# Kernel optimization log

Measured on AMD Instinct MI355X. Metric: run time of the kernel, lower is better.

The kernel has to match this reference:

```python
import jax, jax.numpy as jnp
import numpy as np
from jax import lax

T = 6  # max_message_length


def setup_inputs() -> dict:
    key = jax.random.key(0)
    ks = jax.random.split(key, 10)
    B, VIS, H, E, V = 8192, 512, 256, 64, 4096
    s = lambda k, shp, fan: jax.random.normal(k, shp, jnp.float32) * (1.0 / np.sqrt(fan))
    return {
        "vision_feat": jax.random.normal(ks[0], (B, VIS), jnp.float32),
        "Wv": s(ks[1], (VIS, H), VIS),
        "bv": jnp.zeros((H,), jnp.float32),
        "gru_kernel": s(ks[2], (E, 3 * H), E),          # input kernel [z|r|h]
        "gru_rec_kernel": s(ks[3], (H, 3 * H), H),      # recurrent kernel [z|r|h]
        "gru_bias_in": jnp.zeros((3 * H,), jnp.float32),
        "gru_bias_rec": jnp.zeros((3 * H,), jnp.float32),
        "Wo": s(ks[4], (H, V), H),
        "bo": jnp.zeros((V,), jnp.float32),
        "emb": s(ks[5], (V, E), E),
    }


def _gru_cell(x, h, k, rk, b_in, b_rec):
    # Keras GRUCell, reset_after=True
    H = h.shape[1]
    xm = x @ k + b_in          # [B, 3H]
    hm = h @ rk + b_rec        # [B, 3H]
    xz, xr, xh = xm[:, :H], xm[:, H:2 * H], xm[:, 2 * H:]
    hz, hr, hh = hm[:, :H], hm[:, H:2 * H], hm[:, 2 * H:]
    z = jax.nn.sigmoid(xz + hz)
    r = jax.nn.sigmoid(xr + hr)
    hh_t = jnp.tanh(xh + r * hh)
    return z * h + (1.0 - z) * hh_t


def reference(vision_feat, Wv, bv, gru_kernel, gru_rec_kernel, gru_bias_in,
              gru_bias_rec, Wo, bo, emb):
    B = vision_feat.shape[0]
    # NOTE: original code never feeds h_t back as GRU state; state is fixed.
    prev_hidden = vision_feat @ Wv + bv            # [B, H]
    cell0 = jnp.zeros((B, emb.shape[1]), vision_feat.dtype)

    def step(cell_input, _):
        h = _gru_cell(cell_input, prev_hidden, gru_kernel, gru_rec_kernel,
                      gru_bias_in, gru_bias_rec)
        lp = jax.nn.log_softmax(h @ Wo + bo, axis=1)      # [B, V]
        ent = -jnp.sum(lp * jnp.exp(lp), axis=1)          # [B]
        sym = jnp.argmax(lp, axis=1)                      # greedy (training=False)
        sel = jnp.take_along_axis(lp, sym[:, None], axis=1)[:, 0]
        return emb[sym], (sym, sel, ent, h)

    _, (syms, sels, ents, hs) = lax.scan(step, cell0, None, length=T)
    sequence = syms.T.astype(jnp.float32)                 # [B, T]
    logits = sels.T                                       # [B, T]
    entropy = jnp.mean(ents, axis=0)                      # [B]
    message_length = jnp.full((B,), float(T), jnp.float32)
    h_t = hs[-1]                                          # [B, H]
    return sequence, logits, entropy, message_length, h_t
```

## Files before the change

kernel.cpp:

```cpp
#include <hip/hip_runtime.h>
#include <hip/hip_fp16.h>
#include <math.h>


typedef __attribute__((ext_vector_type(8))) _Float16 half8v;
typedef __attribute__((ext_vector_type(4))) float f32x4;

__device__ __forceinline__ int lds_off(int row, int slot) {
    return (row << 6) + ((slot ^ (row & 3) ^ ((row >> 2) & 3)) << 4);
}

__device__ __forceinline__ void gld_lds16(const void* src, void* dst) {
    __builtin_amdgcn_global_load_lds(
        (const __attribute__((address_space(1))) void*)src,
        (__attribute__((address_space(3))) void*)dst, 16, 0, 0);
}

template<int C>
__device__ __forceinline__ float dppf(float x) {
    return __builtin_bit_cast(float, __builtin_amdgcn_update_dpp(
        __builtin_bit_cast(int, x), __builtin_bit_cast(int, x), C, 0xF, 0xF, false));
}
template<int C>
__device__ __forceinline__ int dppi(int x) {
    return __builtin_amdgcn_update_dpp(x, x, C, 0xF, 0xF, false);
}

__device__ __forceinline__ void f16split(float v, unsigned short& u0,
                                         unsigned short& u1) {
    __half a = __float2half(v);
    float f = __half2float(a);
    __half b = __float2half(v - f);
    u0 = __half_as_ushort(a);
    u1 = __half_as_ushort(b);
}

__device__ __forceinline__ float fast_tanh(float x) {
    float t = __expf(-2.0f * fabsf(x));
    float th = (1.0f - t) / (1.0f + t);
    return copysignf(th, x);
}

__global__ __launch_bounds__(256) void split_ew(
    const float* __restrict__ in, unsigned short* __restrict__ o0,
    unsigned short* __restrict__ o1, int n4)
{
    int i = blockIdx.x * 256 + threadIdx.x;
    if (i >= n4) return;
    float4 v = *(const float4*)&in[(size_t)i * 4];
    unsigned short a[4], b[4];
    f16split(v.x, a[0], b[0]); f16split(v.y, a[1], b[1]);
    f16split(v.z, a[2], b[2]); f16split(v.w, a[3], b[3]);
    *(uint2*)&o0[(size_t)i * 4] = *(uint2*)a;
    *(uint2*)&o1[(size_t)i * 4] = *(uint2*)b;
}

__global__ __launch_bounds__(256) void trans_split(
    const float* __restrict__ W, unsigned short* __restrict__ o0,
    unsigned short* __restrict__ o1, int N, int K)
{
    __shared__ float Ts[64][65];
    const int tid = threadIdx.x;
    const int n0 = blockIdx.x * 64, k0 = blockIdx.y * 64;
    const int ty = tid >> 2, tx = tid & 3;
    #pragma unroll
    for (int q = 0; q < 4; ++q) {
        float4 v = *(const float4*)&W[(size_t)(k0 + ty) * N + n0 + tx * 16 + q * 4];
        Ts[ty][tx * 16 + q * 4 + 0] = v.x; Ts[ty][tx * 16 + q * 4 + 1] = v.y;
        Ts[ty][tx * 16 + q * 4 + 2] = v.z; Ts[ty][tx * 16 + q * 4 + 3] = v.w;
    }
    __syncthreads();
    #pragma unroll
    for (int ii = 0; ii < 2; ++ii) {
        int item = tid + (ii << 8);
        int n = item >> 3, g = item & 7;
        unsigned short u0[8], u1[8];
        #pragma unroll
        for (int e = 0; e < 8; ++e)
            f16split(Ts[g * 8 + e][n], u0[e], u1[e]);
        size_t base = (size_t)(n0 + n) * K + k0 + g * 8;
        *(uint4*)&o0[base] = *(uint4*)u0;
        *(uint4*)&o1[base] = *(uint4*)u1;
    }
}

template<int KTOT, bool SPLIT>
__global__ __launch_bounds__(256) void mfma_gemm(
    const unsigned short* __restrict__ a0s, const unsigned short* __restrict__ a1s,
    const unsigned short* __restrict__ b0s, const unsigned short* __restrict__ b1s,
    const float* __restrict__ bias, float* __restrict__ C, int ldc,
    unsigned short* __restrict__ s0, unsigned short* __restrict__ s1)
{
    __shared__ char lds[16384];
    const int tid = threadIdx.x;
    const int w = tid >> 6, lane = tid & 63;
    const int c16 = lane & 15, rg = lane >> 4;
    const int m0 = blockIdx.y << 6, n0 = blockIdx.x << 6;
    const int arow0 = (w >> 1) << 5, brow0 = (w & 1) << 5;

    const unsigned short* segsrc = (w == 0) ? a0s : (w == 1) ? a1s
                                 : (w == 2) ? b0s : b1s;
    const int segrow0 = (w < 2) ? m0 : n0;

    f32x4 acc[2][2] = {};

    for (int t = 0; t < KTOT / 32; ++t) {
        const int k0 = t << 5;
        #pragma unroll
        for (int q = 0; q < 4; ++q) {
            int row = (q << 4) + (lane >> 2);
            int slot = (lane & 3) ^ (row & 3) ^ ((row >> 2) & 3);
            gld_lds16(segsrc + (size_t)(segrow0 + row) * KTOT + k0 + (slot << 3),
                      &lds[(w << 12) + (q << 10)]);
        }
        asm volatile("s_waitcnt vmcnt(0)" ::: "memory");
        __syncthreads();
        half8v afr[2][2], bfr[2][2];
        #pragma unroll
        for (int i = 0; i < 2; ++i) {
            int oa = lds_off(arow0 + (i << 4) + c16, rg);
            afr[i][0] = *(half8v*)&lds[oa];
            afr[i][1] = *(half8v*)&lds[4096 + oa];
            int ob = lds_off(brow0 + (i << 4) + c16, rg);
            bfr[i][0] = *(half8v*)&lds[8192 + ob];
            bfr[i][1] = *(half8v*)&lds[12288 + ob];
        }
        #pragma unroll
        for (int i = 0; i < 2; ++i)
            #pragma unroll
            for (int j = 0; j < 2; ++j) {
                f32x4 c = acc[i][j];
                c = __builtin_amdgcn_mfma_f32_16x16x32_f16(afr[i][0], bfr[j][0], c, 0, 0, 0);
                c = __builtin_amdgcn_mfma_f32_16x16x32_f16(afr[i][1], bfr[j][0], c, 0, 0, 0);
                c = __builtin_amdgcn_mfma_f32_16x16x32_f16(afr[i][0], bfr[j][1], c, 0, 0, 0);
                acc[i][j] = c;
            }
        __syncthreads();
    }

    #pragma unroll
    for (int j = 0; j < 2; ++j) {
        int col = n0 + brow0 + (j << 4) + c16;
        float bb = bias[col];
        #pragma unroll
        for (int i = 0; i < 2; ++i)
            #pragma unroll
            for (int reg = 0; reg < 4; ++reg) {
                int row = m0 + arow0 + (i << 4) + (rg << 2) + reg;
                float v = acc[i][j][reg] + bb;
                C[(size_t)row * ldc + col] = v;
                if (SPLIT) {
                    unsigned short u0, u1;
                    f16split(v, u0, u1);
                    s0[(size_t)row * ldc + col] = u0;
                    s1[(size_t)row * ldc + col] = u1;
                }
            }
    }
}

__global__ __launch_bounds__(256) void gru_fused(
    const float4* __restrict__ pstats, const float* __restrict__ emb,
    const float* __restrict__ gk, const float* __restrict__ b_in,
    const float* __restrict__ hm, const float* __restrict__ ph,
    unsigned short* __restrict__ h0, unsigned short* __restrict__ h1,
    float* __restrict__ ht_out, float* __restrict__ out_seq,
    float* __restrict__ out_sel, float* __restrict__ out_ent, int t)
{
    __shared__ float xsT[64][8];
    __shared__ int syms_lds[8];
    const int tid = threadIdx.x;
    const int row0 = blockIdx.x * 8;
    float az[8], ar[8], ah[8];
    const float bz = b_in[tid], br = b_in[256 + tid], bh = b_in[512 + tid];
    #pragma unroll
    for (int r = 0; r < 8; ++r) { az[r] = bz; ar[r] = br; ah[r] = bh; }

    if (t > 0) {
        const int r = tid >> 5, p = tid & 31;
        const int row = row0 + r;
        float4 pa = pstats[(size_t)p * 8192 + row];
        float4 pb = pstats[(size_t)(p + 32) * 8192 + row];
        float M = pa.x, S = pa.y + pb.y, Q = pa.z + pb.z;
        int A = __float_as_int(pa.w);
        { int a2 = __float_as_int(pb.w);
          if (pb.x > M || (pb.x == M && a2 < A)) { M = pb.x; A = a2; } }
        #pragma unroll
        for (int off = 1; off < 32; off <<= 1) {
            float m2 = __shfl_xor(M, off);
            float s2 = __shfl_xor(S, off);
            float q2 = __shfl_xor(Q, off);
            int   a2 = __shfl_xor(A, off);
            S += s2; Q += q2;
            if (m2 > M || (m2 == M && a2 < A)) { M = m2; A = a2; }
        }
        if (p == 0) {
            float lse = __logf(S);
            float sel = M - lse;
            float ent = lse - Q / S;
            out_seq[(size_t)row * 6 + (t - 1)] = (float)A;
            out_sel[(size_t)row * 6 + (t - 1)] = sel;
            float ea = (t == 1) ? ent : (out_ent[row] + ent);
            out_ent[row] = ea;
            syms_lds[r] = A;
        }
        __syncthreads();
        for (int l = tid; l < 512; l += 256) {
            int r2 = l >> 6, e = l & 63;
            xsT[e][r2] = emb[(size_t)syms_lds[r2] * 64 + e];
        }
        __syncthreads();
        #pragma unroll 4
        for (int e = 0; e < 64; ++e) {
            float kz  = gk[e * 768 + tid];
            float kr_ = gk[e * 768 + 256 + tid];
            float kh  = gk[e * 768 + 512 + tid];
            float4 x0 = *(float4*)&xsT[e][0];
            float4 x1 = *(float4*)&xsT[e][4];
            float xv[8] = {x0.x, x0.y, x0.z, x0.w, x1.x, x1.y, x1.z, x1.w};
            #pragma unroll
            for (int r2 = 0; r2 < 8; ++r2) {
                az[r2] = fmaf(xv[r2], kz, az[r2]);
                ar[r2] = fmaf(xv[r2], kr_, ar[r2]);
                ah[r2] = fmaf(xv[r2], kh, ah[r2]);
            }
        }
    }
    #pragma unroll
    for (int r = 0; r < 8; ++r) {
        const int row = row0 + r;
        float hz  = hm[(size_t)row * 768 + tid];
        float hr  = hm[(size_t)row * 768 + 256 + tid];
        float hh  = hm[(size_t)row * 768 + 512 + tid];
        float phv = ph[(size_t)row * 256 + tid];
        float z  = 1.0f / (1.0f + __expf(-(az[r] + hz)));
        float rr = 1.0f / (1.0f + __expf(-(ar[r] + hr)));
        float ht = fast_tanh(ah[r] + rr * hh);
        float hv = z * phv + (1.0f - z) * ht;
        size_t idx = (size_t)row * 256 + tid;
        unsigned short u0, u1;
        f16split(hv, u0, u1);
        h0[idx] = u0; h1[idx] = u1;
        if (ht_out) ht_out[idx] = hv;
    }
}

__global__ __launch_bounds__(256, 3) void logits_mfma(
    const unsigned short* __restrict__ h0, const unsigned short* __restrict__ h1,
    const unsigned short* __restrict__ w0, const unsigned short* __restrict__ w1,
    const float* __restrict__ bo, float4* __restrict__ pstats)
{
    __shared__ char lds[32768];
    const int tid = threadIdx.x;
    const int w = tid >> 6, lane = tid & 63;
    const int c16 = lane & 15, rg = lane >> 4;
    const int m0 = blockIdx.y << 7, n0 = blockIdx.x << 7;
    const int arow0 = (w >> 1) << 6, brow0 = (w & 1) << 6;

    const unsigned short* segsrc = (w == 0) ? h0 : (w == 1) ? h1
                                 : (w == 2) ? w0 : w1;
    const int segrow0 = (w < 2) ? m0 : n0;

    f32x4 acc[4][4] = {};

    for (int t = 0; t < 8; ++t) {
        const int k0 = t << 5;
        #pragma unroll
        for (int q = 0; q < 8; ++q) {
            int row = (q << 4) + (lane >> 2);
            int slot = (lane & 3) ^ (row & 3) ^ ((row >> 2) & 3);
            gld_lds16(segsrc + (size_t)(segrow0 + row) * 256 + k0 + (slot << 3),
                      &lds[(w << 13) + (q << 10)]);
        }
        asm volatile("s_waitcnt vmcnt(0)" ::: "memory");
        __syncthreads();
        half8v afr[4][2];
        #pragma unroll
        for (int i = 0; i < 4; ++i) {
            int o = lds_off(arow0 + (i << 4) + c16, rg);
            afr[i][0] = *(half8v*)&lds[o];
            afr[i][1] = *(half8v*)&lds[8192 + o];
        }
        #pragma unroll
        for (int j = 0; j < 4; ++j) {
            int o = lds_off(brow0 + (j << 4) + c16, rg);
            half8v b0 = *(half8v*)&lds[16384 + o];
            half8v b1 = *(half8v*)&lds[24576 + o];
            #pragma unroll
            for (int i = 0; i < 4; ++i) {
                f32x4 c = acc[i][j];
                c = __builtin_amdgcn_mfma_f32_16x16x32_f16(afr[i][0], b0, c, 0, 0, 0);
                c = __builtin_amdgcn_mfma_f32_16x16x32_f16(afr[i][1], b0, c, 0, 0, 0);
                c = __builtin_amdgcn_mfma_f32_16x16x32_f16(afr[i][0], b1, c, 0, 0, 0);
                acc[i][j] = c;
            }
        }
        __syncthreads();
    }

    const int wn0 = n0 + brow0;
    float bov[4];
    #pragma unroll
    for (int j = 0; j < 4; ++j) bov[j] = bo[wn0 + j * 16 + c16];
    #pragma unroll
    for (int i = 0; i < 4; ++i) {
        #pragma unroll
        for (int reg = 0; reg < 4; ++reg) {
            float l0 = acc[i][0][reg] + bov[0];
            float l1 = acc[i][1][reg] + bov[1];
            float l2 = acc[i][2][reg] + bov[2];
            float l3 = acc[i][3][reg] + bov[3];
            float m = l0; int a = wn0 + c16;
            if (l1 > m) { m = l1; a = wn0 + 16 + c16; }
            if (l2 > m) { m = l2; a = wn0 + 32 + c16; }
            if (l3 > m) { m = l3; a = wn0 + 48 + c16; }
            float e0 = __expf(l0), e1 = __expf(l1), e2 = __expf(l2), e3 = __expf(l3);
            float s = (e0 + e1) + (e2 + e3);
            float q = fmaf(l0, e0, fmaf(l1, e1, fmaf(l2, e2, l3 * e3)));
            s += dppf<0x108>(s); s += dppf<0x104>(s);
            s += dppf<0x102>(s); s += dppf<0x101>(s);
            q += dppf<0x108>(q); q += dppf<0x104>(q);
            q += dppf<0x102>(q); q += dppf<0x101>(q);
            #define MMERGE(C) { float m2 = dppf<C>(m); int a2 = dppi<C>(a); \
                bool bt = (m2 > m) || (m2 == m && a2 < a); \
                m = bt ? m2 : m; a = bt ? a2 : a; }
            MMERGE(0x108) MMERGE(0x104) MMERGE(0x102) MMERGE(0x101)
            #undef MMERGE
            if (c16 == 0) {
                int grow = m0 + arow0 + (i << 4) + (rg << 2) + reg;
                pstats[(size_t)((blockIdx.x << 1) + (w & 1)) * 8192 + grow] =
                    make_float4(m, s, q, __int_as_float(a));
            }
        }
    }
}

__global__ __launch_bounds__(64) void finalize_kernel(
    const float4* __restrict__ pstats, float* __restrict__ out_seq,
    float* __restrict__ out_sel, float* __restrict__ out_ent,
    float* __restrict__ out_ml)
{
    const int row = blockIdx.x * 64 + threadIdx.x;
    float M = -INFINITY, S = 0.f, Q = 0.f; int A = 0;
    #pragma unroll 8
    for (int p = 0; p < 64; ++p) {
        float4 pp = pstats[(size_t)p * 8192 + row];
        S += pp.y; Q += pp.z;
        int a2 = __float_as_int(pp.w);
        if (pp.x > M || (pp.x == M && a2 < A)) { M = pp.x; A = a2; }
    }
    float lse = __logf(S);
    float sel = M - lse;
    float ent = lse - Q / S;
    out_seq[(size_t)row * 6 + 5] = (float)A;
    out_sel[(size_t)row * 6 + 5] = sel;
    out_ent[row] = (out_ent[row] + ent) * (1.0f / 6.0f);
    out_ml[row] = 6.0f;
}

extern "C" void kernel_launch(void* const* d_in, const int* in_sizes, int n_in,
                              void* d_out, int out_size, void* d_ws, size_t ws_size,
                              hipStream_t stream) {
    const float* vis  = (const float*)d_in[0];
    const float* Wv   = (const float*)d_in[1];
    const float* bv   = (const float*)d_in[2];
    const float* gk   = (const float*)d_in[3];
    const float* grk  = (const float*)d_in[4];
    const float* bin  = (const float*)d_in[5];
    const float* brec = (const float*)d_in[6];
    const float* Wo   = (const float*)d_in[7];
    const float* bo   = (const float*)d_in[8];
    const float* emb  = (const float*)d_in[9];

    float* out = (float*)d_out;
    float* out_seq = out;
    float* out_sel = out + 49152;
    float* out_ent = out + 98304;
    float* out_ml  = out + 106496;
    float* out_ht  = out + 114688;

    char* ws = (char*)d_ws;
    float*          ph     = (float*)(ws);
    float*          hm     = (float*)(ws + 8388608);
    unsigned short* vis0   = (unsigned short*)(ws + 8388608);
    unsigned short* vis1   = (unsigned short*)(ws + 16777216);
    unsigned short* h0     = (unsigned short*)(ws + 33554432);
    unsigned short* h1     = (unsigned short*)(ws + 37748736);
    unsigned short* w0     = (unsigned short*)(ws + 41943040);
    unsigned short* w1     = (unsigned short*)(ws + 44040192);
    float4*         pstats = (float4*)(ws + 46137344);
    unsigned short* ph0    = (unsigned short*)(ws + 46137344);
    unsigned short* ph1    = (unsigned short*)(ws + 50331648);
    unsigned short* wv0    = (unsigned short*)(ws + 54558720);
    unsigned short* wv1    = (unsigned short*)(ws + 54820864);
    unsigned short* g0     = (unsigned short*)(ws + 55083008);
    unsigned short* g1     = (unsigned short*)(ws + 55476224);

    trans_split<<<dim3(64, 4), 256, 0, stream>>>(Wo, w0, w1, 4096, 256);
    trans_split<<<dim3(4, 8), 256, 0, stream>>>(Wv, wv0, wv1, 256, 512);
    trans_split<<<dim3(12, 4), 256, 0, stream>>>(grk, g0, g1, 768, 256);
    split_ew<<<4096, 256, 0, stream>>>(vis, vis0, vis1, 1048576);

    mfma_gemm<512, true><<<dim3(4, 128), 256, 0, stream>>>(
        vis0, vis1, wv0, wv1, bv, ph, 256, ph0, ph1);
    mfma_gemm<256, false><<<dim3(12, 128), 256, 0, stream>>>(
        ph0, ph1, g0, g1, brec, hm, 768, nullptr, nullptr);

    for (int t = 0; t < 6; ++t) {
        gru_fused<<<1024, 256, 0, stream>>>(pstats, emb, gk, bin, hm, ph,
                                            h0, h1,
                                            (t == 5) ? out_ht : nullptr,
                                            out_seq, out_sel, out_ent, t);
        logits_mfma<<<dim3(32, 64), 256, 0, stream>>>(h0, h1, w0, w1, bo, pstats);
    }
    finalize_kernel<<<128, 64, 0, stream>>>(pstats, out_seq, out_sel,
                                            out_ent, out_ml);
}
```

Baseline: 556.9 us.

## Precompute embedding-times-input-kernel table and gather rows in the GRU step

Adds a one-time MFMA GEMM that computes emb @ gru_kernel into a 4096x768 table in workspace. Each GRU step then gathers the row for the chosen symbol instead of running the 64-deep FMA loop over the embedding. This removes the per-step input projection arithmetic and its LDS staging, but adds an extra GEMM, split kernels and about 25 MB of scattered row reads per step. The new path only runs when the workspace is large enough, and it reuses the h0/h1 buffers as scratch for the split embedding.

```diff
diff --git a/kernel.cpp b/kernel.cpp
--- a/kernel.cpp
+++ b/kernel.cpp
@@ -141,7 +141,7 @@
     #pragma unroll
     for (int j = 0; j < 2; ++j) {
         int col = n0 + brow0 + (j << 4) + c16;
-        float bb = bias[col];
+        float bb = bias ? bias[col] : 0.0f;
         #pragma unroll
         for (int i = 0; i < 2; ++i)
             #pragma unroll
@@ -161,6 +161,7 @@
 
 __global__ __launch_bounds__(256) void gru_fused(
     const float4* __restrict__ pstats, const float* __restrict__ emb,
+    const float* __restrict__ embgk,
     const float* __restrict__ gk, const float* __restrict__ b_in,
     const float* __restrict__ hm, const float* __restrict__ ph,
     unsigned short* __restrict__ h0, unsigned short* __restrict__ h1,
@@ -205,24 +206,34 @@
             syms_lds[r] = A;
         }
         __syncthreads();
-        for (int l = tid; l < 512; l += 256) {
-            int r2 = l >> 6, e = l & 63;
-            xsT[e][r2] = emb[(size_t)syms_lds[r2] * 64 + e];
-        }
-        __syncthreads();
-        #pragma unroll 4
-        for (int e = 0; e < 64; ++e) {
-            float kz  = gk[e * 768 + tid];
-            float kr_ = gk[e * 768 + 256 + tid];
-            float kh  = gk[e * 768 + 512 + tid];
-            float4 x0 = *(float4*)&xsT[e][0];
-            float4 x1 = *(float4*)&xsT[e][4];
-            float xv[8] = {x0.x, x0.y, x0.z, x0.w, x1.x, x1.y, x1.z, x1.w};
+        if (embgk) {
             #pragma unroll
             for (int r2 = 0; r2 < 8; ++r2) {
-                az[r2] = fmaf(xv[r2], kz, az[r2]);
-                ar[r2] = fmaf(xv[r2], kr_, ar[r2]);
-                ah[r2] = fmaf(xv[r2], kh, ah[r2]);
+                size_t b = (size_t)syms_lds[r2] * 768 + tid;
+                az[r2] += embgk[b];
+                ar[r2] += embgk[b + 256];
+                ah[r2] += embgk[b + 512];
+            }
+        } else {
+            for (int l = tid; l < 512; l += 256) {
+                int r2 = l >> 6, e = l & 63;
+                xsT[e][r2] = emb[(size_t)syms_lds[r2] * 64 + e];
+            }
+            __syncthreads();
+            #pragma unroll 4
+            for (int e = 0; e < 64; ++e) {
+                float kz  = gk[e * 768 + tid];
+                float kr_ = gk[e * 768 + 256 + tid];
+                float kh  = gk[e * 768 + 512 + tid];
+                float4 x0 = *(float4*)&xsT[e][0];
+                float4 x1 = *(float4*)&xsT[e][4];
+                float xv[8] = {x0.x, x0.y, x0.z, x0.w, x1.x, x1.y, x1.z, x1.w};
+                #pragma unroll
+                for (int r2 = 0; r2 < 8; ++r2) {
+                    az[r2] = fmaf(xv[r2], kz, az[r2]);
+                    ar[r2] = fmaf(xv[r2], kr_, ar[r2]);
+                    ah[r2] = fmaf(xv[r2], kh, ah[r2]);
+                }
             }
         }
     }
@@ -395,20 +406,35 @@
     unsigned short* wv1    = (unsigned short*)(ws + 54820864);
     unsigned short* g0     = (unsigned short*)(ws + 55083008);
     unsigned short* g1     = (unsigned short*)(ws + 55476224);
+    float*          embgk  = (float*)(ws + 55869440);
+    unsigned short* gk0    = (unsigned short*)(ws + 68452352);
+    unsigned short* gk1    = (unsigned short*)(ws + 68550656);
+
+    const bool use_tbl = (ws_size >= 68648960ULL);
+    unsigned short* emb0 = h0;
+    unsigned short* emb1 = h1;
 
     trans_split<<<dim3(64, 4), 256, 0, stream>>>(Wo, w0, w1, 4096, 256);
     trans_split<<<dim3(4, 8), 256, 0, stream>>>(Wv, wv0, wv1, 256, 512);
     trans_split<<<dim3(12, 4), 256, 0, stream>>>(grk, g0, g1, 768, 256);
     split_ew<<<4096, 256, 0, stream>>>(vis, vis0, vis1, 1048576);
+    if (use_tbl) {
+        trans_split<<<dim3(12, 1), 256, 0, stream>>>(gk, gk0, gk1, 768, 64);
+        split_ew<<<256, 256, 0, stream>>>(emb, emb0, emb1, 65536);
+    }
 
     mfma_gemm<512, true><<<dim3(4, 128), 256, 0, stream>>>(
         vis0, vis1, wv0, wv1, bv, ph, 256, ph0, ph1);
     mfma_gemm<256, false><<<dim3(12, 128), 256, 0, stream>>>(
         ph0, ph1, g0, g1, brec, hm, 768, nullptr, nullptr);
+    if (use_tbl)
+        mfma_gemm<64, false><<<dim3(12, 64), 256, 0, stream>>>(
+            emb0, emb1, gk0, gk1, nullptr, embgk, 768, nullptr, nullptr);
 
     for (int t = 0; t < 6; ++t) {
-        gru_fused<<<1024, 256, 0, stream>>>(pstats, emb, gk, bin, hm, ph,
-                                            h0, h1,
+        gru_fused<<<1024, 256, 0, stream>>>(pstats, emb,
+                                            use_tbl ? embgk : nullptr,
+                                            gk, bin, hm, ph, h0, h1,
                                             (t == 5) ? out_ht : nullptr,
                                             out_seq, out_sel, out_ent, t);
         logits_mfma<<<dim3(32, 64), 256, 0, stream>>>(h0, h1, w0, w1, bo, pstats);
```

After: 520.1 us (median of 2 runs). 6.6% less time.
